# Kernel tuning notes

Measured on AMD Instinct MI355X. Metric: run time of the kernel, lower is better.

Reference implementation:

```python
import jax, jax.numpy as jnp
import numpy as np


def setup_inputs() -> dict:
    key = jax.random.key(0)
    ks = jax.random.split(key, 6)
    B, N, D_in, D, Dg, H = 32, 256, 512, 256, 256, 512
    s = lambda f_in: 1.0 / np.sqrt(f_in)
    return {
        "xi": jax.random.normal(ks[0], (B, N, D_in), dtype=jnp.float32),
        "W_img": jax.random.normal(ks[1], (D_in, D), dtype=jnp.float32) * s(D_in),
        "b_img": jnp.zeros((D,), jnp.float32),
        "W_gnn_self": jax.random.normal(ks[2], (D, Dg), dtype=jnp.float32) * s(D),
        "W_gnn_nbr": jax.random.normal(ks[3], (D, Dg), dtype=jnp.float32) * s(D),
        "b_gnn": jnp.zeros((Dg,), jnp.float32),
        "W1": jax.random.normal(ks[4], (N * Dg, H), dtype=jnp.float32) * s(N * Dg),
        "b1": jnp.zeros((H,), jnp.float32),
        "W2": jax.random.normal(ks[5], (H, 1), dtype=jnp.float32) * s(H),
        "b2": jnp.zeros((1,), jnp.float32),
        "k": 10,
    }


def _knn_edges(xie, k):
    # xie: [B, N, D]. Per-image squared euclidean cdist + top-k (exclude self).
    B, N, _ = xie.shape
    x2 = jnp.sum(xie * xie, axis=-1)  # [B, N]
    d2 = x2[:, :, None] + x2[:, None, :] - 2.0 * jnp.einsum("bnd,bmd->bnm", xie, xie)
    big = jnp.asarray(1e30, d2.dtype)
    d2 = d2 + big * jnp.eye(N, dtype=d2.dtype)  # exclude self
    _, nbr = jax.lax.top_k(-d2, k)  # [B, N, k] neighbor (source) indices
    tgt = jnp.broadcast_to(jnp.arange(N)[None, :, None], (B, N, k))
    return nbr, tgt


def reference(xi, W_img, b_img, W_gnn_self, W_gnn_nbr, b_gnn, W1, b1, W2, b2, k):
    B, N, _ = xi.shape
    # image encoder -> per-node embeddings [B, N, D]
    xie = xi @ W_img + b_img
    # KNN graph build per image, then shift indices into one batched graph
    nbr, tgt = _knn_edges(xie, k)
    shift = (jnp.arange(B) * N)[:, None, None]
    src = (nbr + shift).reshape(-1)  # [B*N*k]
    dst = (tgt + shift).reshape(-1)  # [B*N*k]
    # batched graph conv: mean neighbor aggregation + self transform
    x_flat = xie.reshape(B * N, -1)
    agg = jax.ops.segment_sum(x_flat[src], dst, num_segments=B * N) / k
    gep = jax.nn.relu(x_flat @ W_gnn_self + agg @ W_gnn_nbr + b_gnn)
    gep = gep.reshape(B, N, -1)  # split_batch_graph
    # estimation MLP on flattened graph embedding
    h = jax.nn.relu(gep.reshape(B, -1) @ W1 + b1)
    out = h @ W2 + b2  # [B, 1]
    return xie, gep, out
```

## Files before the change

### kernel.cpp

```cpp
#include <hip/hip_runtime.h>

#define BB 32
#define NN 256
#define DIN 512
#define DD 256
#define HH 512
#define MM 8192
#define NDG 65536
#define KSTR 16

typedef __attribute__((ext_vector_type(8))) __bf16 bf16x8;
typedef __attribute__((ext_vector_type(4))) float f32x4;

__device__ __forceinline__ unsigned short f2bf(float x) {
  unsigned u = __float_as_uint(x);
  u += 0x7FFFu + ((u >> 16) & 1u);
  return (unsigned short)(u >> 16);
}

__global__ __launch_bounds__(256) void k_enc(const float* __restrict__ A,
                                             const float* __restrict__ W,
                                             const float* __restrict__ bias,
                                             float* __restrict__ C) {
  __shared__ float As[16][68];
  __shared__ float Bs[16][68];
  const int tid = threadIdx.x;
  const int m0 = blockIdx.x * 64, n0 = blockIdx.y * 64;
  const int tx = tid & 15, ty = tid >> 4;
  const int lrow = tid >> 2, lfc = (tid & 3) * 4;
  float acc[4][4] = {};
  for (int k0 = 0; k0 < DIN; k0 += 16) {
    float4 va = *reinterpret_cast<const float4*>(&A[(m0 + lrow) * DIN + k0 + lfc]);
    As[lfc + 0][lrow] = va.x; As[lfc + 1][lrow] = va.y;
    As[lfc + 2][lrow] = va.z; As[lfc + 3][lrow] = va.w;
    const int bk = tid >> 4, bn = (tid & 15) * 4;
    *reinterpret_cast<float4*>(&Bs[bk][bn]) =
        *reinterpret_cast<const float4*>(&W[(k0 + bk) * DD + n0 + bn]);
    __syncthreads();
#pragma unroll
    for (int kk = 0; kk < 16; ++kk) {
      float a[4], b[4];
      *reinterpret_cast<float4*>(a) = *reinterpret_cast<float4*>(&As[kk][ty * 4]);
      *reinterpret_cast<float4*>(b) = *reinterpret_cast<float4*>(&Bs[kk][tx * 4]);
#pragma unroll
      for (int i = 0; i < 4; ++i)
#pragma unroll
        for (int j = 0; j < 4; ++j) acc[i][j] += a[i] * b[j];
    }
    __syncthreads();
  }
#pragma unroll
  for (int i = 0; i < 4; ++i) {
    const int m = m0 + ty * 4 + i;
    float4 v;
    v.x = acc[i][0] + bias[n0 + tx * 4 + 0];
    v.y = acc[i][1] + bias[n0 + tx * 4 + 1];
    v.z = acc[i][2] + bias[n0 + tx * 4 + 2];
    v.w = acc[i][3] + bias[n0 + tx * 4 + 3];
    *reinterpret_cast<float4*>(&C[m * DD + n0 + tx * 4]) = v;
  }
}

__global__ __launch_bounds__(256) void k_norm(const float* __restrict__ X,
                                              float* __restrict__ x2) {
  const int tid = threadIdx.x;
  const int row = blockIdx.x * 4 + (tid >> 6);
  const int lane = tid & 63;
  float4 v = *reinterpret_cast<const float4*>(&X[row * DD + lane * 4]);
  float s = v.x * v.x + v.y * v.y + v.z * v.z + v.w * v.w;
#pragma unroll
  for (int off = 1; off < 64; off <<= 1) s += __shfl_xor(s, off);
  if (lane == 0) x2[row] = s;
}

__global__ __launch_bounds__(256) void k_dist(const float* __restrict__ X,
                                              const float* __restrict__ x2,
                                              float* __restrict__ d2) {
  __shared__ float As[16][68];
  __shared__ float Bs[16][68];
  const int tid = threadIdx.x;
  const int b = blockIdx.z;
  const int m0 = blockIdx.x * 64, n0 = blockIdx.y * 64;
  const float* Xb = X + b * NN * DD;
  const int tx = tid & 15, ty = tid >> 4;
  const int lrow = tid >> 2, lfc = (tid & 3) * 4;
  float acc[4][4] = {};
  for (int k0 = 0; k0 < DD; k0 += 16) {
    float4 va = *reinterpret_cast<const float4*>(&Xb[(n0 + lrow) * DD + k0 + lfc]);
    As[lfc + 0][lrow] = va.x; As[lfc + 1][lrow] = va.y;
    As[lfc + 2][lrow] = va.z; As[lfc + 3][lrow] = va.w;
    float4 vb = *reinterpret_cast<const float4*>(&Xb[(m0 + lrow) * DD + k0 + lfc]);
    Bs[lfc + 0][lrow] = vb.x; Bs[lfc + 1][lrow] = vb.y;
    Bs[lfc + 2][lrow] = vb.z; Bs[lfc + 3][lrow] = vb.w;
    __syncthreads();
#pragma unroll
    for (int kk = 0; kk < 16; ++kk) {
      float a[4], bv[4];
      *reinterpret_cast<float4*>(a) = *reinterpret_cast<float4*>(&As[kk][ty * 4]);
      *reinterpret_cast<float4*>(bv) = *reinterpret_cast<float4*>(&Bs[kk][tx * 4]);
#pragma unroll
      for (int i = 0; i < 4; ++i)
#pragma unroll
        for (int j = 0; j < 4; ++j) acc[i][j] += a[i] * bv[j];
    }
    __syncthreads();
  }
#pragma unroll
  for (int i = 0; i < 4; ++i) {
    const int n = n0 + ty * 4 + i;
    const float xn = x2[b * NN + n];
    float4 v;
    float* vv = reinterpret_cast<float*>(&v);
#pragma unroll
    for (int j = 0; j < 4; ++j) {
      const int mc = m0 + tx * 4 + j;
      float dv = xn + x2[b * NN + mc] - 2.0f * acc[i][j];
      if (n == mc) dv = 1e30f;
      vv[j] = dv;
    }
    *reinterpret_cast<float4*>(&d2[(b * NN + n) * NN + m0 + tx * 4]) = v;
  }
}

__global__ __launch_bounds__(256) void k_topk(const float* __restrict__ d2,
                                              const int* __restrict__ kp,
                                              int* __restrict__ nbr) {
  const int tid = threadIdx.x;
  const int i = blockIdx.x * 4 + (tid >> 6);
  const int lane = tid & 63;
  const int kcnt = kp[0];
  const float* row = d2 + (size_t)i * NN;
  float v0 = row[lane];
  float v1 = row[lane + 64];
  float v2 = row[lane + 128];
  float v3 = row[lane + 192];
  for (int it = 0; it < kcnt; ++it) {
    float v = v0; int idx = lane;
    if (v1 < v) { v = v1; idx = lane + 64; }
    if (v2 < v) { v = v2; idx = lane + 128; }
    if (v3 < v) { v = v3; idx = lane + 192; }
#pragma unroll
    for (int off = 1; off < 64; off <<= 1) {
      float ov = __shfl_xor(v, off);
      int oi = __shfl_xor(idx, off);
      if (ov < v || (ov == v && oi < idx)) { v = ov; idx = oi; }
    }
    if (lane == 0) nbr[i * KSTR + it] = idx;
    const int slot = idx >> 6;
    if (lane == (idx & 63)) {
      if (slot == 0) v0 = 3e38f;
      else if (slot == 1) v1 = 3e38f;
      else if (slot == 2) v2 = 3e38f;
      else v3 = 3e38f;
    }
  }
}

__global__ __launch_bounds__(256) void k_agg(const float* __restrict__ X,
                                             const int* __restrict__ nbr,
                                             const int* __restrict__ kp,
                                             unsigned short* __restrict__ A_bf) {
  const int i = blockIdx.x;
  const int b = i >> 8;
  const int t = threadIdx.x;
  const int kcnt = kp[0];
  float acc = 0.0f;
  for (int j = 0; j < kcnt; ++j) {
    const int nb = nbr[i * KSTR + j];
    acc += X[(b * NN + nb) * DD + t];
  }
  A_bf[(size_t)i * 512 + 256 + t] = f2bf(acc / (float)kcnt);
}

__global__ __launch_bounds__(256) void k_cvtx(const float* __restrict__ X,
                                              unsigned short* __restrict__ A_bf) {
  const int qid = blockIdx.x * 256 + threadIdx.x;
  const int m = qid >> 6;
  const int dq = (qid & 63) * 4;
  float4 v = *reinterpret_cast<const float4*>(&X[(size_t)m * DD + dq]);
  ushort4 o;
  o.x = f2bf(v.x); o.y = f2bf(v.y); o.z = f2bf(v.z); o.w = f2bf(v.w);
  *reinterpret_cast<ushort4*>(&A_bf[(size_t)m * 512 + dq]) = o;
}

__global__ __launch_bounds__(256) void k_cvtw(const float* __restrict__ Ws,
                                              const float* __restrict__ Wn,
                                              unsigned short* __restrict__ B_bfT) {
  const int id = blockIdx.x * 256 + threadIdx.x;
  const int k = id >> 8;
  const int n = id & 255;
  float v = (k < 256) ? Ws[k * 256 + n] : Wn[(k - 256) * 256 + n];
  B_bfT[(size_t)n * 512 + k] = f2bf(v);
}

__global__ __launch_bounds__(256) void k_gnn(const unsigned short* __restrict__ A_bf,
                                             const unsigned short* __restrict__ B_bfT,
                                             const float* __restrict__ bias,
                                             float* __restrict__ C) {
  __shared__ unsigned short As[64 * 72];
  __shared__ unsigned short Bs[64 * 72];
  const int tid = threadIdx.x;
  const int m0 = blockIdx.x * 64, n0 = blockIdx.y * 64;
  const int l = tid & 63, w = tid >> 6;
  const int mw = (w & 1) * 32, nw = (w >> 1) * 32;
  const int lr = tid >> 3, lq = tid & 7;
  f32x4 acc[2][2] = {};
  for (int kt = 0; kt < 8; ++kt) {
    const int kb = kt * 64;
#pragma unroll
    for (int s = 0; s < 2; ++s) {
      const int r = lr + s * 32;
      uint4 va = *reinterpret_cast<const uint4*>(&A_bf[(size_t)(m0 + r) * 512 + kb + lq * 8]);
      *reinterpret_cast<uint4*>(&As[r * 72 + lq * 8]) = va;
      uint4 vb = *reinterpret_cast<const uint4*>(&B_bfT[(size_t)(n0 + r) * 512 + kb + lq * 8]);
      *reinterpret_cast<uint4*>(&Bs[r * 72 + lq * 8]) = vb;
    }
    __syncthreads();
#pragma unroll
    for (int ks = 0; ks < 2; ++ks) {
      bf16x8 af[2], bf[2];
#pragma unroll
      for (int mi = 0; mi < 2; ++mi)
        af[mi] = *reinterpret_cast<const bf16x8*>(
            &As[(mw + mi * 16 + (l & 15)) * 72 + ks * 32 + (l >> 4) * 8]);
#pragma unroll
      for (int ni = 0; ni < 2; ++ni)
        bf[ni] = *reinterpret_cast<const bf16x8*>(
            &Bs[(nw + ni * 16 + (l & 15)) * 72 + ks * 32 + (l >> 4) * 8]);
#pragma unroll
      for (int mi = 0; mi < 2; ++mi)
#pragma unroll
        for (int ni = 0; ni < 2; ++ni)
          acc[mi][ni] = __builtin_amdgcn_mfma_f32_16x16x32_bf16(af[mi], bf[ni],
                                                                acc[mi][ni], 0, 0, 0);
    }
    __syncthreads();
  }
#pragma unroll
  for (int mi = 0; mi < 2; ++mi) {
    const int row_base = m0 + mw + mi * 16 + (l >> 4) * 4;
#pragma unroll
    for (int ni = 0; ni < 2; ++ni) {
      const int col = n0 + nw + ni * 16 + (l & 15);
      const float bv = bias[col];
#pragma unroll
      for (int r = 0; r < 4; ++r) {
        float v = acc[mi][ni][r] + bv;
        C[(size_t)(row_base + r) * 256 + col] = v > 0.0f ? v : 0.0f;
      }
    }
  }
}

__global__ __launch_bounds__(512) void k_mlp1(const float* __restrict__ A,
                                              const float* __restrict__ W1,
                                              float* __restrict__ part) {
  __shared__ float lds[8192];
  const int tid = threadIdx.x;
  const int b = blockIdx.x;
  const int k0 = b * 256;
  const int team = tid >> 7;
  const int cq = tid & 127;
  float4 acc[32];
#pragma unroll
  for (int m = 0; m < 32; ++m) acc[m] = make_float4(0.f, 0.f, 0.f, 0.f);

  auto STAGE = [&](int h) {
#pragma unroll
    for (int i = 0; i < 2; ++i) {
      int q = tid + i * 512;
      int m = q >> 5;
      int kq = q & 31;
      float4 v = *reinterpret_cast<const float4*>(
          &A[(size_t)m * 65536 + k0 + h * 128 + kq * 4]);
      float* dst = &lds[h * 4096 + (kq * 4) * 32 + m];
      dst[0] = v.x; dst[32] = v.y; dst[64] = v.z; dst[96] = v.w;
    }
  };

  STAGE(0);
  __syncthreads();
  STAGE(1);

  for (int h = 0; h < 2; ++h) {
    if (h == 1) __syncthreads();
    const int kk0 = team * 32;
    const size_t wbase = ((size_t)(k0 + h * 128 + kk0)) * 512 + cq * 4;
    float4 wA = *reinterpret_cast<const float4*>(&W1[wbase]);
    float4 wB = *reinterpret_cast<const float4*>(&W1[wbase + 512]);
    for (int i = 0; i < 32; i += 2) {
      float4 wC, wD;
      if (i + 2 < 32) {
        wC = *reinterpret_cast<const float4*>(&W1[wbase + (size_t)(i + 2) * 512]);
        wD = *reinterpret_cast<const float4*>(&W1[wbase + (size_t)(i + 3) * 512]);
      }
      const float4* A4a = reinterpret_cast<const float4*>(&lds[h * 4096 + (kk0 + i) * 32]);
      const float4* A4b = reinterpret_cast<const float4*>(&lds[h * 4096 + (kk0 + i + 1) * 32]);
#pragma unroll
      for (int m8 = 0; m8 < 8; ++m8) {
        float4 av = A4a[m8];
        acc[m8 * 4 + 0].x += av.x * wA.x; acc[m8 * 4 + 0].y += av.x * wA.y;
        acc[m8 * 4 + 0].z += av.x * wA.z; acc[m8 * 4 + 0].w += av.x * wA.w;
        acc[m8 * 4 + 1].x += av.y * wA.x; acc[m8 * 4 + 1].y += av.y * wA.y;
        acc[m8 * 4 + 1].z += av.y * wA.z; acc[m8 * 4 + 1].w += av.y * wA.w;
        acc[m8 * 4 + 2].x += av.z * wA.x; acc[m8 * 4 + 2].y += av.z * wA.y;
        acc[m8 * 4 + 2].z += av.z * wA.z; acc[m8 * 4 + 2].w += av.z * wA.w;
        acc[m8 * 4 + 3].x += av.w * wA.x; acc[m8 * 4 + 3].y += av.w * wA.y;
        acc[m8 * 4 + 3].z += av.w * wA.z; acc[m8 * 4 + 3].w += av.w * wA.w;
      }
#pragma unroll
      for (int m8 = 0; m8 < 8; ++m8) {
        float4 av = A4b[m8];
        acc[m8 * 4 + 0].x += av.x * wB.x; acc[m8 * 4 + 0].y += av.x * wB.y;
        acc[m8 * 4 + 0].z += av.x * wB.z; acc[m8 * 4 + 0].w += av.x * wB.w;
        acc[m8 * 4 + 1].x += av.y * wB.x; acc[m8 * 4 + 1].y += av.y * wB.y;
        acc[m8 * 4 + 1].z += av.y * wB.z; acc[m8 * 4 + 1].w += av.y * wB.w;
        acc[m8 * 4 + 2].x += av.z * wB.x; acc[m8 * 4 + 2].y += av.z * wB.y;
        acc[m8 * 4 + 2].z += av.z * wB.z; acc[m8 * 4 + 2].w += av.z * wB.w;
        acc[m8 * 4 + 3].x += av.w * wB.x; acc[m8 * 4 + 3].y += av.w * wB.y;
        acc[m8 * 4 + 3].z += av.w * wB.z; acc[m8 * 4 + 3].w += av.w * wB.w;
      }
      wA = wC; wB = wD;
    }
  }

  float4* lds4 = reinterpret_cast<float4*>(lds);
  for (int rg = 0; rg < 8; ++rg) {
    __syncthreads();
    if (team > 0) {
#pragma unroll
      for (int r = 0; r < 4; ++r)
        lds4[(team - 1) * 512 + r * 128 + cq] = acc[rg * 4 + r];
    }
    __syncthreads();
    if (team == 0) {
#pragma unroll
      for (int r = 0; r < 4; ++r) {
        float4 s = acc[rg * 4 + r];
        float4 p0 = lds4[r * 128 + cq];
        float4 p1 = lds4[512 + r * 128 + cq];
        float4 p2 = lds4[1024 + r * 128 + cq];
        s.x += p0.x + p1.x + p2.x; s.y += p0.y + p1.y + p2.y;
        s.z += p0.z + p1.z + p2.z; s.w += p0.w + p1.w + p2.w;
        *reinterpret_cast<float4*>(
            &part[((size_t)b * 32 + rg * 4 + r) * 512 + cq * 4]) = s;
      }
    }
  }
}

__global__ __launch_bounds__(256) void k_mlp1r(const float* __restrict__ part,
                                               const float* __restrict__ b1,
                                               float* __restrict__ h) {
  __shared__ float red[3][64];
  const int tid = threadIdx.x;
  const int m = blockIdx.x >> 3;
  const int c = (blockIdx.x & 7) * 64 + (tid & 63);
  const int bq = tid >> 6;
  float s = 0.0f;
  for (int bb = bq * 64; bb < bq * 64 + 64; ++bb)
    s += part[((size_t)bb * 32 + m) * 512 + c];
  if (bq > 0) red[bq - 1][tid & 63] = s;
  __syncthreads();
  if (bq == 0) {
    s += red[0][tid & 63] + red[1][tid & 63] + red[2][tid & 63];
    s += b1[c];
    h[m * HH + c] = s > 0.0f ? s : 0.0f;
  }
}

__global__ __launch_bounds__(256) void k_out(const float* __restrict__ h,
                                             const float* __restrict__ W2,
                                             const float* __restrict__ b2,
                                             float* __restrict__ outp) {
  const int tid = threadIdx.x;
  const int m = blockIdx.x * 4 + (tid >> 6);
  const int lane = tid & 63;
  float s = 0.0f;
#pragma unroll
  for (int j = 0; j < 8; ++j) s += h[m * HH + lane + 64 * j] * W2[lane + 64 * j];
#pragma unroll
  for (int off = 1; off < 64; off <<= 1) s += __shfl_xor(s, off);
  if (lane == 0) outp[m] = s + b2[0];
}

extern "C" void kernel_launch(void* const* d_in, const int* in_sizes, int n_in,
                              void* d_out, int out_size, void* d_ws, size_t ws_size,
                              hipStream_t stream) {
  const float* xi     = (const float*)d_in[0];
  const float* W_img  = (const float*)d_in[1];
  const float* b_img  = (const float*)d_in[2];
  const float* W_self = (const float*)d_in[3];
  const float* W_nbr  = (const float*)d_in[4];
  const float* b_gnn  = (const float*)d_in[5];
  const float* W1     = (const float*)d_in[6];
  const float* b1     = (const float*)d_in[7];
  const float* W2     = (const float*)d_in[8];
  const float* b2     = (const float*)d_in[9];
  const int*   kp     = (const int*)d_in[10];

  float* xie  = (float*)d_out;
  float* gep  = xie + (size_t)MM * DD;
  float* outp = gep + (size_t)MM * DD;

  float* ws   = (float*)d_ws;
  float* x2   = ws;
  int*   nbr  = (int*)(ws + MM);
  float* d2   = ws + MM + MM * KSTR;
  float* part = d2 + (size_t)MM * DD;
  float* hbuf = part + (size_t)256 * 32 * HH;
  unsigned short* A_bf  = (unsigned short*)(hbuf + BB * HH);
  unsigned short* B_bfT = A_bf + (size_t)MM * 512;

  k_enc  <<<dim3(128, 4), 256, 0, stream>>>(xi, W_img, b_img, xie);
  k_cvtw <<<512, 256, 0, stream>>>(W_self, W_nbr, B_bfT);
  k_norm <<<MM / 4, 256, 0, stream>>>(xie, x2);
  k_dist <<<dim3(4, 4, BB), 256, 0, stream>>>(xie, x2, d2);
  k_topk <<<MM / 4, 256, 0, stream>>>(d2, kp, nbr);
  k_cvtx <<<2048, 256, 0, stream>>>(xie, A_bf);
  k_agg  <<<MM, 256, 0, stream>>>(xie, nbr, kp, A_bf);
  k_gnn  <<<dim3(128, 4), 256, 0, stream>>>(A_bf, B_bfT, b_gnn, gep);
  k_mlp1 <<<256, 512, 0, stream>>>(gep, W1, part);
  k_mlp1r<<<256, 256, 0, stream>>>(part, b1, hbuf);
  k_out  <<<8, 256, 0, stream>>>(hbuf, W2, b2, outp);
}
```

Before: 167.1 us.

## Restructure encoder GEMM with split-K teams, fuse bf16 convert, widen MLP1 blocks

The encoder GEMM now stages a full 32-row slab of the input in LDS and streams W_img from global memory with register prefetch. Two teams split K and reduce through LDS, and the kernel writes the bf16 copy of xie directly, which removes the separate k_cvtx kernel and its extra pass over xie. k_mlp1 moves to 1024-thread blocks where two row halves each hold 16 accumulators instead of 32, cutting register pressure and keeping the A tile in row-major LDS. The risks are a large LDS footprint in k_enc (about 66 KB per block), which limits occupancy, and W_img being re-read from global by every block.

```diff
diff --git a/kernel.cpp b/kernel.cpp
--- a/kernel.cpp
+++ b/kernel.cpp
@@ -18,46 +18,81 @@
   return (unsigned short)(u >> 16);
 }
 
-__global__ __launch_bounds__(256) void k_enc(const float* __restrict__ A,
-                                             const float* __restrict__ W,
-                                             const float* __restrict__ bias,
-                                             float* __restrict__ C) {
-  __shared__ float As[16][68];
-  __shared__ float Bs[16][68];
-  const int tid = threadIdx.x;
-  const int m0 = blockIdx.x * 64, n0 = blockIdx.y * 64;
-  const int tx = tid & 15, ty = tid >> 4;
-  const int lrow = tid >> 2, lfc = (tid & 3) * 4;
-  float acc[4][4] = {};
-  for (int k0 = 0; k0 < DIN; k0 += 16) {
-    float4 va = *reinterpret_cast<const float4*>(&A[(m0 + lrow) * DIN + k0 + lfc]);
-    As[lfc + 0][lrow] = va.x; As[lfc + 1][lrow] = va.y;
-    As[lfc + 2][lrow] = va.z; As[lfc + 3][lrow] = va.w;
-    const int bk = tid >> 4, bn = (tid & 15) * 4;
-    *reinterpret_cast<float4*>(&Bs[bk][bn]) =
-        *reinterpret_cast<const float4*>(&W[(k0 + bk) * DD + n0 + bn]);
-    __syncthreads();
-#pragma unroll
-    for (int kk = 0; kk < 16; ++kk) {
-      float a[4], b[4];
-      *reinterpret_cast<float4*>(a) = *reinterpret_cast<float4*>(&As[kk][ty * 4]);
-      *reinterpret_cast<float4*>(b) = *reinterpret_cast<float4*>(&Bs[kk][tx * 4]);
-#pragma unroll
-      for (int i = 0; i < 4; ++i)
-#pragma unroll
-        for (int j = 0; j < 4; ++j) acc[i][j] += a[i] * b[j];
-    }
-    __syncthreads();
-  }
-#pragma unroll
-  for (int i = 0; i < 4; ++i) {
-    const int m = m0 + ty * 4 + i;
-    float4 v;
-    v.x = acc[i][0] + bias[n0 + tx * 4 + 0];
-    v.y = acc[i][1] + bias[n0 + tx * 4 + 1];
-    v.z = acc[i][2] + bias[n0 + tx * 4 + 2];
-    v.w = acc[i][3] + bias[n0 + tx * 4 + 3];
-    *reinterpret_cast<float4*>(&C[m * DD + n0 + tx * 4]) = v;
+__global__ __launch_bounds__(256, 4) void k_enc(const float* __restrict__ A,
+                                                const float* __restrict__ W,
+                                                const float* __restrict__ bias,
+                                                float* __restrict__ C,
+                                                unsigned short* __restrict__ A_bf) {
+  __shared__ float Asm[32][516];
+  const int tid = threadIdx.x;
+  const int mb0 = blockIdx.x * 32;
+  const int cq = tid & 63;
+  const int team = (tid >> 6) & 1;
+  const int mh = tid >> 7;
+#pragma unroll
+  for (int i = 0; i < 16; ++i) {
+    int idx = tid + i * 256;
+    int m = idx >> 7;
+    int kq = idx & 127;
+    float4 v = *reinterpret_cast<const float4*>(&A[(size_t)(mb0 + m) * DIN + kq * 4]);
+    *reinterpret_cast<float4*>(&Asm[m][kq * 4]) = v;
+  }
+  __syncthreads();
+  float4 acc[16];
+#pragma unroll
+  for (int m = 0; m < 16; ++m) acc[m] = make_float4(0.f, 0.f, 0.f, 0.f);
+  const int kt0 = team * 256;
+  const float* wp = &W[(size_t)kt0 * DD + cq * 4];
+  float4 wc[4], wn[4];
+#pragma unroll
+  for (int j = 0; j < 4; ++j)
+    wc[j] = *reinterpret_cast<const float4*>(&wp[(size_t)j * DD]);
+  for (int it = 0; it < 64; ++it) {
+    if (it < 63) {
+#pragma unroll
+      for (int j = 0; j < 4; ++j)
+        wn[j] = *reinterpret_cast<const float4*>(&wp[(size_t)((it + 1) * 4 + j) * DD]);
+    }
+    const int kk = kt0 + it * 4;
+#pragma unroll
+    for (int m = 0; m < 16; ++m) {
+      float4 a = *reinterpret_cast<const float4*>(&Asm[mh * 16 + m][kk]);
+      acc[m].x += a.x * wc[0].x; acc[m].y += a.x * wc[0].y;
+      acc[m].z += a.x * wc[0].z; acc[m].w += a.x * wc[0].w;
+      acc[m].x += a.y * wc[1].x; acc[m].y += a.y * wc[1].y;
+      acc[m].z += a.y * wc[1].z; acc[m].w += a.y * wc[1].w;
+      acc[m].x += a.z * wc[2].x; acc[m].y += a.z * wc[2].y;
+      acc[m].z += a.z * wc[2].z; acc[m].w += a.z * wc[2].w;
+      acc[m].x += a.w * wc[3].x; acc[m].y += a.w * wc[3].y;
+      acc[m].z += a.w * wc[3].z; acc[m].w += a.w * wc[3].w;
+    }
+#pragma unroll
+    for (int j = 0; j < 4; ++j) wc[j] = wn[j];
+  }
+  float* red = &Asm[0][0];
+  __syncthreads();
+  if (team == 1) {
+#pragma unroll
+    for (int m = 0; m < 16; ++m)
+      *reinterpret_cast<float4*>(&red[(mh * 16 + m) * 256 + cq * 4]) = acc[m];
+  }
+  __syncthreads();
+  if (team == 0) {
+    float4 bv = *reinterpret_cast<const float4*>(&bias[cq * 4]);
+#pragma unroll
+    for (int m = 0; m < 16; ++m) {
+      float4 o = *reinterpret_cast<float4*>(&red[(mh * 16 + m) * 256 + cq * 4]);
+      float4 s;
+      s.x = acc[m].x + o.x + bv.x;
+      s.y = acc[m].y + o.y + bv.y;
+      s.z = acc[m].z + o.z + bv.z;
+      s.w = acc[m].w + o.w + bv.w;
+      const int row = mb0 + mh * 16 + m;
+      *reinterpret_cast<float4*>(&C[(size_t)row * DD + cq * 4]) = s;
+      ushort4 ob;
+      ob.x = f2bf(s.x); ob.y = f2bf(s.y); ob.z = f2bf(s.z); ob.w = f2bf(s.w);
+      *reinterpret_cast<ushort4*>(&A_bf[(size_t)row * 512 + cq * 4]) = ob;
+    }
   }
 }
 
@@ -172,17 +207,6 @@
   A_bf[(size_t)i * 512 + 256 + t] = f2bf(acc / (float)kcnt);
 }
 
-__global__ __launch_bounds__(256) void k_cvtx(const float* __restrict__ X,
-                                              unsigned short* __restrict__ A_bf) {
-  const int qid = blockIdx.x * 256 + threadIdx.x;
-  const int m = qid >> 6;
-  const int dq = (qid & 63) * 4;
-  float4 v = *reinterpret_cast<const float4*>(&X[(size_t)m * DD + dq]);
-  ushort4 o;
-  o.x = f2bf(v.x); o.y = f2bf(v.y); o.z = f2bf(v.z); o.w = f2bf(v.w);
-  *reinterpret_cast<ushort4*>(&A_bf[(size_t)m * 512 + dq]) = o;
-}
-
 __global__ __launch_bounds__(256) void k_cvtw(const float* __restrict__ Ws,
                                               const float* __restrict__ Wn,
                                               unsigned short* __restrict__ B_bfT) {
@@ -252,98 +276,76 @@
   }
 }
 
-__global__ __launch_bounds__(512) void k_mlp1(const float* __restrict__ A,
-                                              const float* __restrict__ W1,
-                                              float* __restrict__ part) {
-  __shared__ float lds[8192];
+__global__ __launch_bounds__(1024, 4) void k_mlp1(const float* __restrict__ A,
+                                                  const float* __restrict__ W1,
+                                                  float* __restrict__ part) {
+  __shared__ float Asm[32][260];
+  __shared__ float4 red[3][4][2][128];
   const int tid = threadIdx.x;
   const int b = blockIdx.x;
   const int k0 = b * 256;
-  const int team = tid >> 7;
   const int cq = tid & 127;
-  float4 acc[32];
-#pragma unroll
-  for (int m = 0; m < 32; ++m) acc[m] = make_float4(0.f, 0.f, 0.f, 0.f);
-
-  auto STAGE = [&](int h) {
-#pragma unroll
-    for (int i = 0; i < 2; ++i) {
-      int q = tid + i * 512;
-      int m = q >> 5;
-      int kq = q & 31;
-      float4 v = *reinterpret_cast<const float4*>(
-          &A[(size_t)m * 65536 + k0 + h * 128 + kq * 4]);
-      float* dst = &lds[h * 4096 + (kq * 4) * 32 + m];
-      dst[0] = v.x; dst[32] = v.y; dst[64] = v.z; dst[96] = v.w;
-    }
-  };
-
-  STAGE(0);
+  const int team = (tid >> 7) & 3;
+  const int mh = tid >> 9;
+#pragma unroll
+  for (int i = 0; i < 2; ++i) {
+    int idx = tid + i * 1024;
+    int m = idx >> 6;
+    int kq = idx & 63;
+    float4 v = *reinterpret_cast<const float4*>(&A[(size_t)m * NDG + k0 + kq * 4]);
+    *reinterpret_cast<float4*>(&Asm[m][kq * 4]) = v;
+  }
   __syncthreads();
-  STAGE(1);
-
-  for (int h = 0; h < 2; ++h) {
-    if (h == 1) __syncthreads();
-    const int kk0 = team * 32;
-    const size_t wbase = ((size_t)(k0 + h * 128 + kk0)) * 512 + cq * 4;
-    float4 wA = *reinterpret_cast<const float4*>(&W1[wbase]);
-    float4 wB = *reinterpret_cast<const float4*>(&W1[wbase + 512]);
-    for (int i = 0; i < 32; i += 2) {
-      float4 wC, wD;
-      if (i + 2 < 32) {
-        wC = *reinterpret_cast<const float4*>(&W1[wbase + (size_t)(i + 2) * 512]);
-        wD = *reinterpret_cast<const float4*>(&W1[wbase + (size_t)(i + 3) * 512]);
-      }
-      const float4* A4a = reinterpret_cast<const float4*>(&lds[h * 4096 + (kk0 + i) * 32]);
-      const float4* A4b = reinterpret_cast<const float4*>(&lds[h * 4096 + (kk0 + i + 1) * 32]);
-#pragma unroll
-      for (int m8 = 0; m8 < 8; ++m8) {
-        float4 av = A4a[m8];
-        acc[m8 * 4 + 0].x += av.x * wA.x; acc[m8 * 4 + 0].y += av.x * wA.y;
-        acc[m8 * 4 + 0].z += av.x * wA.z; acc[m8 * 4 + 0].w += av.x * wA.w;
-        acc[m8 * 4 + 1].x += av.y * wA.x; acc[m8 * 4 + 1].y += av.y * wA.y;
-        acc[m8 * 4 + 1].z += av.y * wA.z; acc[m8 * 4 + 1].w += av.y * wA.w;
-        acc[m8 * 4 + 2].x += av.z * wA.x; acc[m8 * 4 + 2].y += av.z * wA.y;
-        acc[m8 * 4 + 2].z += av.z * wA.z; acc[m8 * 4 + 2].w += av.z * wA.w;
-        acc[m8 * 4 + 3].x += av.w * wA.x; acc[m8 * 4 + 3].y += av.w * wA.y;
-        acc[m8 * 4 + 3].z += av.w * wA.z; acc[m8 * 4 + 3].w += av.w * wA.w;
-      }
-#pragma unroll
-      for (int m8 = 0; m8 < 8; ++m8) {
-        float4 av = A4b[m8];
-        acc[m8 * 4 + 0].x += av.x * wB.x; acc[m8 * 4 + 0].y += av.x * wB.y;
-        acc[m8 * 4 + 0].z += av.x * wB.z; acc[m8 * 4 + 0].w += av.x * wB.w;
-        acc[m8 * 4 + 1].x += av.y * wB.x; acc[m8 * 4 + 1].y += av.y * wB.y;
-        acc[m8 * 4 + 1].z += av.y * wB.z; acc[m8 * 4 + 1].w += av.y * wB.w;
-        acc[m8 * 4 + 2].x += av.z * wB.x; acc[m8 * 4 + 2].y += av.z * wB.y;
-        acc[m8 * 4 + 2].z += av.z * wB.z; acc[m8 * 4 + 2].w += av.z * wB.w;
-        acc[m8 * 4 + 3].x += av.w * wB.x; acc[m8 * 4 + 3].y += av.w * wB.y;
-        acc[m8 * 4 + 3].z += av.w * wB.z; acc[m8 * 4 + 3].w += av.w * wB.w;
-      }
-      wA = wC; wB = wD;
-    }
-  }
-
-  float4* lds4 = reinterpret_cast<float4*>(lds);
-  for (int rg = 0; rg < 8; ++rg) {
+  float4 acc[16];
+#pragma unroll
+  for (int m = 0; m < 16; ++m) acc[m] = make_float4(0.f, 0.f, 0.f, 0.f);
+  const int kt0 = team * 64;
+  const float* wp = &W1[((size_t)k0 + kt0) * HH + cq * 4];
+  float4 wc[4], wn[4];
+#pragma unroll
+  for (int j = 0; j < 4; ++j)
+    wc[j] = *reinterpret_cast<const float4*>(&wp[(size_t)j * HH]);
+  for (int it = 0; it < 16; ++it) {
+    if (it < 15) {
+#pragma unroll
+      for (int j = 0; j < 4; ++j)
+        wn[j] = *reinterpret_cast<const float4*>(&wp[(size_t)((it + 1) * 4 + j) * HH]);
+    }
+    const int kk = kt0 + it * 4;
+#pragma unroll
+    for (int m = 0; m < 16; ++m) {
+      float4 a = *reinterpret_cast<const float4*>(&Asm[mh * 16 + m][kk]);
+      acc[m].x += a.x * wc[0].x; acc[m].y += a.x * wc[0].y;
+      acc[m].z += a.x * wc[0].z; acc[m].w += a.x * wc[0].w;
+      acc[m].x += a.y * wc[1].x; acc[m].y += a.y * wc[1].y;
+      acc[m].z += a.y * wc[1].z; acc[m].w += a.y * wc[1].w;
+      acc[m].x += a.z * wc[2].x; acc[m].y += a.z * wc[2].y;
+      acc[m].z += a.z * wc[2].z; acc[m].w += a.z * wc[2].w;
+      acc[m].x += a.w * wc[3].x; acc[m].y += a.w * wc[3].y;
+      acc[m].z += a.w * wc[3].z; acc[m].w += a.w * wc[3].w;
+    }
+#pragma unroll
+    for (int j = 0; j < 4; ++j) wc[j] = wn[j];
+  }
+#pragma unroll
+  for (int rg = 0; rg < 4; ++rg) {
     __syncthreads();
     if (team > 0) {
 #pragma unroll
-      for (int r = 0; r < 4; ++r)
-        lds4[(team - 1) * 512 + r * 128 + cq] = acc[rg * 4 + r];
+      for (int r = 0; r < 4; ++r) red[team - 1][r][mh][cq] = acc[rg * 4 + r];
     }
     __syncthreads();
     if (team == 0) {
 #pragma unroll
       for (int r = 0; r < 4; ++r) {
         float4 s = acc[rg * 4 + r];
-        float4 p0 = lds4[r * 128 + cq];
-        float4 p1 = lds4[512 + r * 128 + cq];
-        float4 p2 = lds4[1024 + r * 128 + cq];
+        float4 p0 = red[0][r][mh][cq];
+        float4 p1 = red[1][r][mh][cq];
+        float4 p2 = red[2][r][mh][cq];
         s.x += p0.x + p1.x + p2.x; s.y += p0.y + p1.y + p2.y;
         s.z += p0.z + p1.z + p2.z; s.w += p0.w + p1.w + p2.w;
         *reinterpret_cast<float4*>(
-            &part[((size_t)b * 32 + rg * 4 + r) * 512 + cq * 4]) = s;
+            &part[((size_t)b * 32 + mh * 16 + rg * 4 + r) * HH + cq * 4]) = s;
       }
     }
   }
@@ -412,15 +414,14 @@
   unsigned short* A_bf  = (unsigned short*)(hbuf + BB * HH);
   unsigned short* B_bfT = A_bf + (size_t)MM * 512;
 
-  k_enc  <<<dim3(128, 4), 256, 0, stream>>>(xi, W_img, b_img, xie);
+  k_enc  <<<MM / 32, 256, 0, stream>>>(xi, W_img, b_img, xie, A_bf);
   k_cvtw <<<512, 256, 0, stream>>>(W_self, W_nbr, B_bfT);
   k_norm <<<MM / 4, 256, 0, stream>>>(xie, x2);
   k_dist <<<dim3(4, 4, BB), 256, 0, stream>>>(xie, x2, d2);
   k_topk <<<MM / 4, 256, 0, stream>>>(d2, kp, nbr);
-  k_cvtx <<<2048, 256, 0, stream>>>(xie, A_bf);
   k_agg  <<<MM, 256, 0, stream>>>(xie, nbr, kp, A_bf);
   k_gnn  <<<dim3(128, 4), 256, 0, stream>>>(A_bf, B_bfT, b_gnn, gep);
-  k_mlp1 <<<256, 512, 0, stream>>>(gep, W1, part);
+  k_mlp1 <<<256, 1024, 0, stream>>>(gep, W1, part);
   k_mlp1r<<<256, 256, 0, stream>>>(part, b1, hbuf);
   k_out  <<<8, 256, 0, stream>>>(hbuf, W2, b2, outp);
 }
```

Result: no change. 170.2 us (+1.8%).
